# Performance work log

Hardware: AMD Instinct MI355X
Metric: run time of the kernel (lower is better)

The kernel has to match this reference:

```python
import jax, jax.numpy as jnp
import numpy as np

DIM_IN, DIM_Q, DIM_V = 1024, 1024, 1024
B, S = 4, 2048
NEG_INF = 1.0e9


def setup_inputs() -> dict:
    key = jax.random.key(0)
    ks = jax.random.split(key, 11)
    c_q = (6.0 / (DIM_IN + DIM_Q)) ** 0.5
    c_v = (6.0 / (DIM_IN + DIM_V)) ** 0.5
    b_bound = 1.0 / np.sqrt(DIM_IN)  # torch Linear default bias init
    return {
        "query": jax.random.normal(ks[0], (B, S, DIM_IN), jnp.float32),
        "key": jax.random.normal(ks[1], (B, S, DIM_IN), jnp.float32),
        "value": jax.random.normal(ks[2], (B, S, DIM_IN), jnp.float32),
        "mask": jax.random.randint(ks[3], (B, S, S), 0, 2).astype(bool),
        "Wq": jax.random.uniform(ks[4], (DIM_Q, DIM_IN), jnp.float32, -c_q, c_q),
        "bq": jax.random.uniform(ks[5], (DIM_Q,), jnp.float32, -b_bound, b_bound),
        "Wk": jax.random.uniform(ks[6], (DIM_Q, DIM_IN), jnp.float32, -c_q, c_q),
        "bk": jax.random.uniform(ks[7], (DIM_Q,), jnp.float32, -b_bound, b_bound),
        "Wv": jax.random.uniform(ks[8], (DIM_V, DIM_IN), jnp.float32, -c_v, c_v),
        "bv": jax.random.uniform(ks[9], (DIM_V,), jnp.float32, -b_bound, b_bound),
    }


def reference(query, key, value, mask, Wq, bq, Wk, bk, Wv, bv):
    q = jnp.einsum("bsd,qd->bsq", query, Wq) + bq  # [B,S,dim_q]
    k = jnp.einsum("bsd,qd->bsq", key, Wk) + bk    # [B,S,dim_q]
    v = jnp.einsum("bsd,vd->bsv", value, Wv) + bv  # [B,S,dim_v]
    scale = 1.0 / jnp.sqrt(jnp.asarray(q.shape[-1], q.dtype))
    scores = jnp.einsum("bqd,bkd->bqk", q, k) * scale  # [B,S,S]
    scores = jnp.where(mask, -NEG_INF, scores)
    affinity = jax.nn.softmax(scores, axis=-1)
    out = jnp.einsum("bqk,bkv->bqv", affinity, v)  # [B,S,dim_v]
    return out
```

## Files before the change

kernel.cpp:

```cpp
#include <hip/hip_runtime.h>

#define BB 4
#define SS 2048
#define DD 1024

typedef __attribute__((ext_vector_type(8))) short short8;
typedef __attribute__((ext_vector_type(4))) float f32x4;

__device__ __forceinline__ unsigned short f2b(float f) {
  unsigned u = __builtin_bit_cast(unsigned, f);
  u += 0x7fffu + ((u >> 16) & 1u);
  return (unsigned short)(u >> 16);
}

__device__ __forceinline__ void gl2lds16(const void* g, void* l) {
  __builtin_amdgcn_global_load_lds(
      (__attribute__((address_space(1))) unsigned int*)(void*)(size_t)(uintptr_t)g,
      (__attribute__((address_space(3))) unsigned int*)l, 16, 0, 0);
}

__global__ void detect_mask(const unsigned int* __restrict__ m, int* __restrict__ flag) {
  unsigned any = 0;
#pragma unroll
  for (int i = 0; i < 16; ++i) {
    unsigned v = m[threadIdx.x * 16 + i];
    any |= (v > 1u) ? 1u : 0u;
  }
  unsigned long long b = __ballot(any != 0u);
  if (threadIdx.x == 0) *flag = (b != 0ULL) ? 1 : 0;
}

__global__ __launch_bounds__(256) void cvt3(
    const float* __restrict__ s0, const float* __restrict__ s1, const float* __restrict__ s2,
    unsigned short* __restrict__ d0, unsigned short* __restrict__ d1, unsigned short* __restrict__ d2) {
  const float* s = blockIdx.z == 0 ? s0 : (blockIdx.z == 1 ? s1 : s2);
  unsigned short* d = blockIdx.z == 0 ? d0 : (blockIdx.z == 1 ? d1 : d2);
  size_t i = ((size_t)blockIdx.x * 256 + threadIdx.x) * 8;
  float4 a = *(const float4*)(s + i);
  float4 b = *(const float4*)(s + i + 4);
  union { unsigned short us[8]; uint4 v; } o;
  o.us[0] = f2b(a.x); o.us[1] = f2b(a.y); o.us[2] = f2b(a.z); o.us[3] = f2b(a.w);
  o.us[4] = f2b(b.x); o.us[5] = f2b(b.y); o.us[6] = f2b(b.z); o.us[7] = f2b(b.w);
  *(uint4*)(d + i) = o.v;
}

enum { EPI_BIAS_COL = 0, EPI_BIAS_ROW = 1, EPI_MASK = 2, EPI_OUT = 3 };

template <int EPI>
__global__ __launch_bounds__(256, 2) void gemm_bt(
    const unsigned short* __restrict__ A, int lda, long long aBatch,
    const unsigned short* __restrict__ Bm, int ldb, long long bBatch,
    void* __restrict__ Cv, int ldc, long long cBatch,
    int K,
    const float* __restrict__ bias,
    const void* __restrict__ mask, long long maskBatch,
    const int* __restrict__ mflag,
    float scale) {
  __shared__ unsigned short sA[128 * 32];
  __shared__ unsigned short sB[128 * 32];
  const int tid  = threadIdx.x;
  const int wave = tid >> 6;
  const int lane = tid & 63;
  const int l15  = lane & 15;
  const int quad = lane >> 4;
  const int waveR = wave >> 1, waveC = wave & 1;
  const int bm = blockIdx.x * 128;
  const int bn = blockIdx.y * 128;
  const int z  = blockIdx.z;
  A  += (long long)z * aBatch;
  Bm += (long long)z * bBatch;

  const unsigned short* gA0 = A  + (size_t)(bm + (tid >> 2)) * lda + (tid & 3) * 8;
  const unsigned short* gA1 = gA0 + (size_t)64 * lda;
  const unsigned short* gB0 = Bm + (size_t)(bn + (tid >> 2)) * ldb + (tid & 3) * 8;
  const unsigned short* gB1 = gB0 + (size_t)64 * ldb;
  unsigned short* lA = sA + wave * 64 * 8;
  unsigned short* lB = sB + wave * 64 * 8;

  f32x4 acc[4][4] = {};

  const int aro = (waveR * 64 + l15) * 32 + quad * 8;
  const int bro = (waveC * 64 + l15) * 32 + quad * 8;

  for (int kt = 0; kt < K; kt += 32) {
    gl2lds16(gA0, lA);
    gl2lds16(gA1, lA + 256 * 8);
    gl2lds16(gB0, lB);
    gl2lds16(gB1, lB + 256 * 8);
    gA0 += 32; gA1 += 32; gB0 += 32; gB1 += 32;
    __syncthreads();
    short8 af[4], bf[4];
#pragma unroll
    for (int i = 0; i < 4; ++i) af[i] = *(const short8*)(sA + aro + i * 16 * 32);
#pragma unroll
    for (int j = 0; j < 4; ++j) bf[j] = *(const short8*)(sB + bro + j * 16 * 32);
#pragma unroll
    for (int i = 0; i < 4; ++i)
#pragma unroll
      for (int j = 0; j < 4; ++j)
        acc[i][j] = __builtin_amdgcn_mfma_f32_16x16x32_bf16(af[i], bf[j], acc[i][j], 0, 0, 0);
    __syncthreads();
  }

  const int r0 = bm + waveR * 64 + quad * 4;
  const int c0 = bn + waveC * 64 + l15;

  if constexpr (EPI == EPI_MASK) {
    float* Cz = (float*)Cv + (long long)z * cBatch;
    const int isU8 = *mflag;
    const unsigned char* m8 = (const unsigned char*)mask + (long long)z * maskBatch;
    const int* m32 = (const int*)mask + (long long)z * maskBatch;
#pragma unroll
    for (int i = 0; i < 4; ++i)
#pragma unroll
      for (int r = 0; r < 4; ++r) {
        int row = r0 + i * 16 + r;
#pragma unroll
        for (int j = 0; j < 4; ++j) {
          int col = c0 + j * 16;
          size_t idx = (size_t)row * ldc + col;
          float v = acc[i][j][r] * scale;
          int mv = isU8 ? (int)m8[idx] : m32[idx];
          if (mv) v = -1.0e9f;
          Cz[idx] = v;
        }
      }
  } else if constexpr (EPI == EPI_OUT) {
    float* Cz = (float*)Cv + (long long)z * cBatch;
#pragma unroll
    for (int i = 0; i < 4; ++i)
#pragma unroll
      for (int r = 0; r < 4; ++r) {
        int row = r0 + i * 16 + r;
#pragma unroll
        for (int j = 0; j < 4; ++j) {
          int col = c0 + j * 16;
          Cz[(size_t)row * ldc + col] = acc[i][j][r];
        }
      }
  } else {
    unsigned short* Cz = (unsigned short*)Cv + (long long)z * cBatch;
#pragma unroll
    for (int i = 0; i < 4; ++i)
#pragma unroll
      for (int r = 0; r < 4; ++r) {
        int row = r0 + i * 16 + r;
#pragma unroll
        for (int j = 0; j < 4; ++j) {
          int col = c0 + j * 16;
          float v = acc[i][j][r] + (EPI == EPI_BIAS_COL ? bias[col] : bias[row]);
          Cz[(size_t)row * ldc + col] = f2b(v);
        }
      }
  }
}

__global__ __launch_bounds__(256) void softmax_rows(const float* __restrict__ Sc,
                                                    unsigned short* __restrict__ P) {
  const size_t r = blockIdx.x;
  const float* src = Sc + r * SS;
  unsigned short* dst = P + r * SS;
  const int tid = threadIdx.x;
  const int wave = tid >> 6, lane = tid & 63;
  float4 x0 = *(const float4*)(src + tid * 8);
  float4 x1 = *(const float4*)(src + tid * 8 + 4);
  float xs[8] = {x0.x, x0.y, x0.z, x0.w, x1.x, x1.y, x1.z, x1.w};
  float mx = xs[0];
#pragma unroll
  for (int k = 1; k < 8; ++k) mx = fmaxf(mx, xs[k]);
#pragma unroll
  for (int o = 32; o; o >>= 1) mx = fmaxf(mx, __shfl_xor(mx, o));
  __shared__ float red[8];
  if (lane == 0) red[wave] = mx;
  __syncthreads();
  mx = fmaxf(fmaxf(red[0], red[1]), fmaxf(red[2], red[3]));
  float e[8], s = 0.f;
#pragma unroll
  for (int k = 0; k < 8; ++k) { e[k] = __expf(xs[k] - mx); s += e[k]; }
#pragma unroll
  for (int o = 32; o; o >>= 1) s += __shfl_xor(s, o);
  if (lane == 0) red[4 + wave] = s;
  __syncthreads();
  s = (red[4] + red[5]) + (red[6] + red[7]);
  float inv = 1.0f / s;
  union { unsigned short us[8]; uint4 v; } o;
#pragma unroll
  for (int k = 0; k < 8; ++k) o.us[k] = f2b(e[k] * inv);
  *(uint4*)(dst + tid * 8) = o.v;
}

extern "C" void kernel_launch(void* const* d_in, const int* in_sizes, int n_in,
                              void* d_out, int out_size, void* d_ws, size_t ws_size,
                              hipStream_t stream) {
  const float* query = (const float*)d_in[0];
  const float* key   = (const float*)d_in[1];
  const float* value = (const float*)d_in[2];
  const void*  mask  = d_in[3];
  const float* Wq = (const float*)d_in[4];
  const float* bq = (const float*)d_in[5];
  const float* Wk = (const float*)d_in[6];
  const float* bk = (const float*)d_in[7];
  const float* Wv = (const float*)d_in[8];
  const float* bv = (const float*)d_in[9];
  float* out = (float*)d_out;

  char* ws = (char*)d_ws;
  const size_t MB = 1024 * 1024;
  unsigned short* qin = (unsigned short*)(ws + 0 * MB);
  unsigned short* kin = (unsigned short*)(ws + 16 * MB);
  unsigned short* vin = (unsigned short*)(ws + 32 * MB);
  unsigned short* Wqb = (unsigned short*)(ws + 48 * MB);
  unsigned short* Wkb = (unsigned short*)(ws + 50 * MB);
  unsigned short* Wvb = (unsigned short*)(ws + 52 * MB);
  unsigned short* qb  = (unsigned short*)(ws + 54 * MB);
  unsigned short* kb  = (unsigned short*)(ws + 70 * MB);
  unsigned short* vT  = (unsigned short*)(ws + 86 * MB);
  float*          Sc  = (float*)(ws + 102 * MB);
  unsigned short* P   = (unsigned short*)(ws + 166 * MB);
  int*          flag  = (int*)(ws + 198 * MB);

  dim3 blk(256);

  detect_mask<<<dim3(1), dim3(64), 0, stream>>>((const unsigned int*)mask, flag);

  cvt3<<<dim3(4096, 1, 3), blk, 0, stream>>>(query, key, value, qin, kin, vin);
  cvt3<<<dim3(512, 1, 3), blk, 0, stream>>>(Wq, Wk, Wv, Wqb, Wkb, Wvb);

  gemm_bt<EPI_BIAS_COL><<<dim3(64, 8, 1), blk, 0, stream>>>(
      qin, 1024, 0, Wqb, 1024, 0, qb, 1024, 0, 1024, bq, nullptr, 0, flag, 0.f);
  gemm_bt<EPI_BIAS_COL><<<dim3(64, 8, 1), blk, 0, stream>>>(
      kin, 1024, 0, Wkb, 1024, 0, kb, 1024, 0, 1024, bk, nullptr, 0, flag, 0.f);

  gemm_bt<EPI_BIAS_ROW><<<dim3(8, 64, 1), blk, 0, stream>>>(
      Wvb, 1024, 0, vin, 1024, 0, vT, 8192, 0, 1024, bv, nullptr, 0, flag, 0.f);

  gemm_bt<EPI_MASK><<<dim3(16, 16, BB), blk, 0, stream>>>(
      qb, 1024, (long long)SS * 1024, kb, 1024, (long long)SS * 1024,
      Sc, SS, (long long)SS * SS, 1024, nullptr, mask, (long long)SS * SS, flag, 0.03125f);

  softmax_rows<<<dim3(BB * SS), blk, 0, stream>>>(Sc, P);

  gemm_bt<EPI_OUT><<<dim3(16, 8, BB), blk, 0, stream>>>(
      P, SS, (long long)SS * SS, vT, 8192, (long long)SS,
      out, 1024, (long long)SS * 1024, SS, nullptr, nullptr, 0, flag, 1.f);
}
```

Before: 432.7 us.

## Store scores as bf16 and apply a bit-packed mask inside softmax

The score GEMM now writes bf16 scores without a mask, which halves the size of the score buffer. A new kernel packs the boolean mask into one bit per element, and softmax applies that mask while reading the bf16 scores. This moves mask reads out of the strided GEMM epilogue and shrinks traffic for the large B×S×S intermediates. It adds a kernel launch and one full pass over the mask, and rounding the scores to bf16 before softmax costs some precision.

```diff
diff --git a/kernel.cpp b/kernel.cpp
--- a/kernel.cpp
+++ b/kernel.cpp
@@ -12,6 +12,10 @@
   u += 0x7fffu + ((u >> 16) & 1u);
   return (unsigned short)(u >> 16);
 }
+__device__ __forceinline__ float b2f(unsigned short us) {
+  unsigned u = (unsigned)us << 16;
+  return __builtin_bit_cast(float, u);
+}
 
 __device__ __forceinline__ void gl2lds16(const void* g, void* l) {
   __builtin_amdgcn_global_load_lds(
@@ -28,6 +32,29 @@
   }
   unsigned long long b = __ballot(any != 0u);
   if (threadIdx.x == 0) *flag = (b != 0ULL) ? 1 : 0;
+}
+
+__global__ __launch_bounds__(256) void pack_mask(const void* __restrict__ mask,
+                                                 const int* __restrict__ flag,
+                                                 unsigned char* __restrict__ bits) {
+  const size_t row = blockIdx.x;
+  const int t = threadIdx.x;
+  unsigned byte = 0;
+  if (*flag) {
+    uint2 v = *(const uint2*)((const unsigned char*)mask + row * SS + t * 8);
+#pragma unroll
+    for (int j = 0; j < 4; ++j) {
+      byte |= (((v.x >> (8 * j)) & 0xffu) ? 1u : 0u) << j;
+      byte |= (((v.y >> (8 * j)) & 0xffu) ? 1u : 0u) << (j + 4);
+    }
+  } else {
+    const uint4* p = (const uint4*)((const int*)mask + row * SS + t * 8);
+    uint4 a = p[0], b = p[1];
+    byte = (a.x ? 1u : 0u) | ((a.y ? 1u : 0u) << 1) | ((a.z ? 1u : 0u) << 2) |
+           ((a.w ? 1u : 0u) << 3) | ((b.x ? 1u : 0u) << 4) | ((b.y ? 1u : 0u) << 5) |
+           ((b.z ? 1u : 0u) << 6) | ((b.w ? 1u : 0u) << 7);
+  }
+  bits[row * 256 + t] = (unsigned char)byte;
 }
 
 __global__ __launch_bounds__(256) void cvt3(
@@ -44,7 +71,7 @@
   *(uint4*)(d + i) = o.v;
 }
 
-enum { EPI_BIAS_COL = 0, EPI_BIAS_ROW = 1, EPI_MASK = 2, EPI_OUT = 3 };
+enum { EPI_BIAS_COL = 0, EPI_BIAS_ROW = 1, EPI_SCORE = 2, EPI_OUT = 3 };
 
 template <int EPI>
 __global__ __launch_bounds__(256, 2) void gemm_bt(
@@ -53,8 +80,6 @@
     void* __restrict__ Cv, int ldc, long long cBatch,
     int K,
     const float* __restrict__ bias,
-    const void* __restrict__ mask, long long maskBatch,
-    const int* __restrict__ mflag,
     float scale) {
   __shared__ unsigned short sA[128 * 32];
   __shared__ unsigned short sB[128 * 32];
@@ -105,11 +130,8 @@
   const int r0 = bm + waveR * 64 + quad * 4;
   const int c0 = bn + waveC * 64 + l15;
 
-  if constexpr (EPI == EPI_MASK) {
-    float* Cz = (float*)Cv + (long long)z * cBatch;
-    const int isU8 = *mflag;
-    const unsigned char* m8 = (const unsigned char*)mask + (long long)z * maskBatch;
-    const int* m32 = (const int*)mask + (long long)z * maskBatch;
+  if constexpr (EPI == EPI_SCORE) {
+    unsigned short* Cz = (unsigned short*)Cv + (long long)z * cBatch;
 #pragma unroll
     for (int i = 0; i < 4; ++i)
 #pragma unroll
@@ -118,11 +140,7 @@
 #pragma unroll
         for (int j = 0; j < 4; ++j) {
           int col = c0 + j * 16;
-          size_t idx = (size_t)row * ldc + col;
-          float v = acc[i][j][r] * scale;
-          int mv = isU8 ? (int)m8[idx] : m32[idx];
-          if (mv) v = -1.0e9f;
-          Cz[idx] = v;
+          Cz[(size_t)row * ldc + col] = f2b(acc[i][j][r] * scale);
         }
       }
   } else if constexpr (EPI == EPI_OUT) {
@@ -155,16 +173,21 @@
   }
 }
 
-__global__ __launch_bounds__(256) void softmax_rows(const float* __restrict__ Sc,
+__global__ __launch_bounds__(256) void softmax_rows(const unsigned short* __restrict__ Sc,
+                                                    const unsigned char* __restrict__ bits,
                                                     unsigned short* __restrict__ P) {
   const size_t r = blockIdx.x;
-  const float* src = Sc + r * SS;
+  const unsigned short* src = Sc + r * SS;
   unsigned short* dst = P + r * SS;
   const int tid = threadIdx.x;
   const int wave = tid >> 6, lane = tid & 63;
-  float4 x0 = *(const float4*)(src + tid * 8);
-  float4 x1 = *(const float4*)(src + tid * 8 + 4);
-  float xs[8] = {x0.x, x0.y, x0.z, x0.w, x1.x, x1.y, x1.z, x1.w};
+  union { unsigned short us[8]; uint4 v; } in;
+  in.v = *(const uint4*)(src + tid * 8);
+  const unsigned mb = bits[r * 256 + tid];
+  float xs[8];
+#pragma unroll
+  for (int k = 0; k < 8; ++k)
+    xs[k] = ((mb >> k) & 1u) ? -1.0e9f : b2f(in.us[k]);
   float mx = xs[0];
 #pragma unroll
   for (int k = 1; k < 8; ++k) mx = fmaxf(mx, xs[k]);
@@ -215,32 +238,34 @@
   unsigned short* qb  = (unsigned short*)(ws + 54 * MB);
   unsigned short* kb  = (unsigned short*)(ws + 70 * MB);
   unsigned short* vT  = (unsigned short*)(ws + 86 * MB);
-  float*          Sc  = (float*)(ws + 102 * MB);
-  unsigned short* P   = (unsigned short*)(ws + 166 * MB);
-  int*          flag  = (int*)(ws + 198 * MB);
+  unsigned short* Sc  = (unsigned short*)(ws + 102 * MB);
+  unsigned short* P   = (unsigned short*)(ws + 134 * MB);
+  unsigned char*  bits= (unsigned char*)(ws + 166 * MB);
+  int*            flag= (int*)(ws + 168 * MB);
 
   dim3 blk(256);
 
   detect_mask<<<dim3(1), dim3(64), 0, stream>>>((const unsigned int*)mask, flag);
+  pack_mask<<<dim3(BB * SS), blk, 0, stream>>>(mask, flag, bits);
 
   cvt3<<<dim3(4096, 1, 3), blk, 0, stream>>>(query, key, value, qin, kin, vin);
   cvt3<<<dim3(512, 1, 3), blk, 0, stream>>>(Wq, Wk, Wv, Wqb, Wkb, Wvb);
 
   gemm_bt<EPI_BIAS_COL><<<dim3(64, 8, 1), blk, 0, stream>>>(
-      qin, 1024, 0, Wqb, 1024, 0, qb, 1024, 0, 1024, bq, nullptr, 0, flag, 0.f);
+      qin, 1024, 0, Wqb, 1024, 0, qb, 1024, 0, 1024, bq, 0.f);
   gemm_bt<EPI_BIAS_COL><<<dim3(64, 8, 1), blk, 0, stream>>>(
-      kin, 1024, 0, Wkb, 1024, 0, kb, 1024, 0, 1024, bk, nullptr, 0, flag, 0.f);
+      kin, 1024, 0, Wkb, 1024, 0, kb, 1024, 0, 1024, bk, 0.f);
 
   gemm_bt<EPI_BIAS_ROW><<<dim3(8, 64, 1), blk, 0, stream>>>(
-      Wvb, 1024, 0, vin, 1024, 0, vT, 8192, 0, 1024, bv, nullptr, 0, flag, 0.f);
-
-  gemm_bt<EPI_MASK><<<dim3(16, 16, BB), blk, 0, stream>>>(
+      Wvb, 1024, 0, vin, 1024, 0, vT, 8192, 0, 1024, bv, 0.f);
+
+  gemm_bt<EPI_SCORE><<<dim3(16, 16, BB), blk, 0, stream>>>(
       qb, 1024, (long long)SS * 1024, kb, 1024, (long long)SS * 1024,
-      Sc, SS, (long long)SS * SS, 1024, nullptr, mask, (long long)SS * SS, flag, 0.03125f);
-
-  softmax_rows<<<dim3(BB * SS), blk, 0, stream>>>(Sc, P);
+      Sc, SS, (long long)SS * SS, 1024, nullptr, 0.03125f);
+
+  softmax_rows<<<dim3(BB * SS), blk, 0, stream>>>(Sc, bits, P);
 
   gemm_bt<EPI_OUT><<<dim3(16, 8, BB), blk, 0, stream>>>(
       P, SS, (long long)SS * SS, vT, 8192, (long long)SS,
-      out, 1024, (long long)SS * 1024, SS, nullptr, nullptr, 0, flag, 1.f);
-}
+      out, 1024, (long long)SS * 1024, SS, nullptr, 1.f);
+}
```

Result: faster. 397.7 us (-8.1%).
